# Kernel tuning notes

Hardware: AMD Instinct MI355X
Metric: run time of the kernel (lower is better)

Reference implementation:

```python
import jax, jax.numpy as jnp
import numpy as np

N, P = 65536, 1024

def setup_inputs() -> dict:
    key = jax.random.key(0)
    k1, k2, k3, k4 = jax.random.split(key, 4)
    X = jax.random.normal(k1, (N, P), dtype=jnp.float32)
    beta0 = jax.random.normal(k2, (1,), dtype=jnp.float32)
    beta = jax.random.normal(k3, (P,), dtype=jnp.float32)
    Theta = jax.random.normal(k4, (P, P), dtype=jnp.float32)
    return {"X": X, "beta0": beta0, "beta": beta, "Theta": Theta}

def reference(X, beta0, beta, Theta):
    # y_hat = beta0 + X @ beta + sum_{j<k} Theta[j,k] * X[:,j] * X[:,k]
    # The double loop uses only the strictly upper-triangular part of Theta.
    p = Theta.shape[0]
    theta_upper = jnp.triu(Theta, k=1)                     # [p, p]
    linear = beta0 + X @ beta                              # [n]
    interaction = jnp.sum((X @ theta_upper) * X, axis=1)   # [n], quadratic form
    return linear + interaction
```

## Files before the change

kernel.cpp:

```cpp
#include <hip/hip_runtime.h>


typedef __bf16 bf16_t;
typedef bf16_t bf16x8 __attribute__((ext_vector_type(8)));
typedef float f32x4 __attribute__((ext_vector_type(4)));
typedef unsigned short u16;
typedef u16 u16x4 __attribute__((ext_vector_type(4)));
typedef u16 u16x8 __attribute__((ext_vector_type(8)));

#define N_ROWS 65536
#define P_DIM  1024
#define BM 128
#define BN 128
#define BK 32

static __device__ __forceinline__ u16 f2bf(float f) {
  unsigned u = __builtin_bit_cast(unsigned, f);
  u += 0x7FFFu + ((u >> 16) & 1u);
  return (u16)(u >> 16);
}

static __device__ __forceinline__ void gload16(const void* g, void* lds_base) {
  __builtin_amdgcn_global_load_lds(
      (const __attribute__((address_space(1))) unsigned char*)g,
      (__attribute__((address_space(3))) unsigned char*)lds_base, 16, 0, 0);
}

__global__ void __launch_bounds__(256)
init_y(float* __restrict__ y, const float* __restrict__ beta0) {
  int i = blockIdx.x * blockDim.x + threadIdx.x;
  if (i < N_ROWS) y[i] = beta0[0];
}

__global__ void __launch_bounds__(128)
conv_theta(const float* __restrict__ Theta, u16* __restrict__ Tt,
           float* __restrict__ y, const float* __restrict__ beta0) {
  __shared__ float tile[32][33];
  const int tid = threadIdx.x;
  const int tg  = (blockIdx.y * gridDim.x + blockIdx.x) * 128 + tid;
  if (tg < N_ROWS) y[tg] = beta0[0];

  const int k0  = blockIdx.x * 32;
  const int c0  = blockIdx.y * 32;
  {
    const int tx = tid & 31;
    const int rb = tid >> 5;
    #pragma unroll
    for (int i = 0; i < 8; ++i) {
      int kl = rb * 8 + i;
      tile[kl][tx] = Theta[(size_t)(k0 + kl) * P_DIM + c0 + tx];
    }
  }
  __syncthreads();
  {
    const int cl = tid >> 2;
    const int qt = tid & 3;
    const int c  = c0 + cl;
    const int Q  = blockIdx.x * 4 + qt;
    u16x8 w;
    #pragma unroll
    for (int e = 0; e < 8; ++e) {
      int k = Q * 8 + e;
      float v = tile[qt * 8 + e][cl];
      w[e] = (k < c) ? f2bf(v) : (u16)0;
    }
    const int qs = (qt ^ ((c >> 1) & 3));
    *(u16x8*)(Tt + (size_t)c * P_DIM + (size_t)(blockIdx.x * 32 + qs * 8)) = w;
  }
}

__global__ void __launch_bounds__(512)
gemm_r18(const float* __restrict__ X, const u16* __restrict__ Tt,
         const float* __restrict__ beta, float* __restrict__ y)
{
  __shared__ __align__(16) u16 L[20480];

  const int nwg = (N_ROWS / BM) * (P_DIM / BN);
  const int swz = (blockIdx.x & 7) * (nwg / 8) + (blockIdx.x >> 3);
  const int bn  = 7 - (swz & 7);
  const int bm  = swz >> 3;
  const int c0  = bn * BN;
  const int m0  = bm * BM;
  const int nkt = (bn + 1) * 4;

  const int tid  = threadIdx.x;
  const int lane = tid & 63;
  const int wid  = tid >> 6;
  const int wm   = wid >> 1;
  const int wn   = wid & 1;
  const int l15  = lane & 15;
  const int lg   = lane >> 4;

  const int ar = tid >> 2;
  const int ap = tid & 3;
  const int aq = (ap ^ ((ar >> 1) & 3)) * 8;

  const int brow = wid * 16 + (lane >> 2);
  const int bq   = (lane & 3) * 8;

  f32x4 acc[2][4];
  #pragma unroll
  for (int i = 0; i < 2; ++i)
    #pragma unroll
    for (int j = 0; j < 4; ++j)
      acc[i][j] = (f32x4)0.0f;

  f32x4 av0, av1;

  #define STAGE_A_LOAD(t_)                                                      \
    {                                                                           \
      const float* s_ = X + (size_t)(m0 + ar) * P_DIM + (t_) * BK + ap * 8;     \
      av0 = ((const f32x4*)s_)[0];                                              \
      av1 = ((const f32x4*)s_)[1];                                              \
    }
  #define STAGE_A_WRITE(ab_)                                                    \
    {                                                                           \
      u16x8 w_;                                                                 \
      _Pragma("unroll")                                                         \
      for (int j = 0; j < 4; ++j) { w_[j] = f2bf(av0[j]); w_[j + 4] = f2bf(av1[j]); } \
      *(u16x8*)&L[(ab_) * 4096 + ar * 32 + aq] = w_;                            \
    }
  #define STAGE_B(bb_, t_)                                                      \
    gload16(Tt + (size_t)(c0 + brow) * P_DIM + (t_) * BK + bq,                  \
            &L[8192 + (bb_) * 4096 + wid * 512]);

  STAGE_B(0, 0)
  STAGE_B(1, 1)
  STAGE_A_LOAD(0)
  asm volatile("s_waitcnt vmcnt(0)" ::: "memory");
  __builtin_amdgcn_sched_barrier(0);
  STAGE_A_WRITE(0)
  asm volatile("s_waitcnt lgkmcnt(0)" ::: "memory");
  __builtin_amdgcn_sched_barrier(0);
  __builtin_amdgcn_s_barrier();
  __builtin_amdgcn_sched_barrier(0);

  for (int t = 0; t < nkt; ++t) {
    const int acur = t & 1;
    const int bcur = t % 3;
    const bool pre1 = (t + 1 < nkt);
    const bool pre2 = (t + 2 < nkt);
    if (pre1) STAGE_A_LOAD(t + 1)
    if (pre2) STAGE_B((t + 2) % 3, t + 2)

    bf16x8 af[2], bfr[4];
    #pragma unroll
    for (int mi = 0; mi < 2; ++mi) {
      const int rw = wm * 32 + mi * 16 + l15;
      u16x8 v = *(const u16x8*)&L[acur * 4096 + rw * 32 + (lg ^ ((rw >> 1) & 3)) * 8];
      af[mi] = __builtin_bit_cast(bf16x8, v);
    }
    #pragma unroll
    for (int ni = 0; ni < 4; ++ni) {
      const int cl = wn * 64 + ni * 16 + l15;
      u16x8 v = *(const u16x8*)&L[8192 + bcur * 4096 + cl * 32 + (lg ^ ((cl >> 1) & 3)) * 8];
      bfr[ni] = __builtin_bit_cast(bf16x8, v);
    }

    __builtin_amdgcn_s_setprio(1);
    #pragma unroll
    for (int mi = 0; mi < 2; ++mi)
      #pragma unroll
      for (int ni = 0; ni < 4; ++ni)
        acc[mi][ni] = __builtin_amdgcn_mfma_f32_16x16x32_bf16(bfr[ni], af[mi], acc[mi][ni], 0, 0, 0);
    __builtin_amdgcn_s_setprio(0);

    if (pre2) {
      asm volatile("s_waitcnt vmcnt(2)" ::: "memory");
    } else {
      asm volatile("s_waitcnt vmcnt(0)" ::: "memory");
    }
    __builtin_amdgcn_sched_barrier(0);
    if (pre1) STAGE_A_WRITE((t + 1) & 1)
    asm volatile("s_waitcnt lgkmcnt(0)" ::: "memory");
    __builtin_amdgcn_sched_barrier(0);
    __builtin_amdgcn_s_barrier();
    __builtin_amdgcn_sched_barrier(0);
  }
  #undef STAGE_A_LOAD
  #undef STAGE_A_WRITE
  #undef STAGE_B

  float ysum[2];
  ysum[0] = 0.0f; ysum[1] = 0.0f;

  #pragma unroll
  for (int mi = 0; mi < 2; ++mi) {
    const int row = m0 + wm * 32 + mi * 16 + l15;
    const float* xr = X + (size_t)row * P_DIM;
    #pragma unroll
    for (int ni = 0; ni < 4; ++ni) {
      const int cb = c0 + wn * 64 + ni * 16 + lg * 4;
      f32x4 xw = *(const f32x4*)(xr + cb);
      f32x4 bv = *(const f32x4*)(beta + cb);
      #pragma unroll
      for (int r = 0; r < 4; ++r)
        ysum[mi] += (acc[mi][ni][r] + bv[r]) * xw[r];
    }
  }

  #pragma unroll
  for (int mi = 0; mi < 2; ++mi) {
    ysum[mi] += __shfl_xor(ysum[mi], 16);
    ysum[mi] += __shfl_xor(ysum[mi], 32);
  }
  if (lane < 16) {
    #pragma unroll
    for (int mi = 0; mi < 2; ++mi)
      atomicAdd(&y[m0 + wm * 32 + mi * 16 + l15], ysum[mi]);
  }
}

#define LDT 40
__global__ void __launch_bounds__(256)
fused_quad_fallback(const float* __restrict__ X, const float* __restrict__ beta,
                    const float* __restrict__ Theta, float* __restrict__ y)
{
  __shared__ __align__(16) u16 Alds[128 * LDT];
  __shared__ __align__(16) u16 Blds[128 * LDT];

  const int bid = blockIdx.x;
  const int bn  = bid & 7;
  const int bm  = bid >> 3;
  const int c0  = bn * 128;
  const int m0  = bm * 128;
  const int nkt = (bn + 1) * 4;

  const int tid  = threadIdx.x;
  const int lane = tid & 63;
  const int wid  = tid >> 6;
  const int wm   = wid >> 1;
  const int wn   = wid & 1;
  const int l15  = lane & 15;
  const int lg   = lane >> 4;

  f32x4 acc[4][4];
  #pragma unroll
  for (int i = 0; i < 4; ++i)
    #pragma unroll
    for (int j = 0; j < 4; ++j)
      acc[i][j] = (f32x4)0.0f;

  const int arow  = tid >> 1;
  const int ahalf = (tid & 1) * 16;
  const int kb4 = (tid >> 5) * 4;
  const int cb4 = (tid & 31) * 4;

  for (int kt = 0; kt < nkt; ++kt) {
    const int k0 = kt * 32;
    __syncthreads();
    {
      const f32x4* p = (const f32x4*)(X + (size_t)(m0 + arow) * P_DIM + k0 + ahalf);
      f32x4 v0 = p[0], v1 = p[1], v2 = p[2], v3 = p[3];
      u16x8 w0, w1;
      #pragma unroll
      for (int i = 0; i < 4; ++i) {
        w0[i] = f2bf(v0[i]); w0[i + 4] = f2bf(v1[i]);
        w1[i] = f2bf(v2[i]); w1[i + 4] = f2bf(v3[i]);
      }
      *(u16x8*)&Alds[arow * LDT + ahalf]     = w0;
      *(u16x8*)&Alds[arow * LDT + ahalf + 8] = w1;
    }
    {
      float e[4][4];
      #pragma unroll
      for (int i = 0; i < 4; ++i) {
        f32x4 r = *(const f32x4*)(Theta + (size_t)(k0 + kb4 + i) * P_DIM + c0 + cb4);
        #pragma unroll
        for (int j = 0; j < 4; ++j)
          e[i][j] = ((k0 + kb4 + i) < (c0 + cb4 + j)) ? r[j] : 0.0f;
      }
      #pragma unroll
      for (int j = 0; j < 4; ++j) {
        u16x4 wv;
        #pragma unroll
        for (int i = 0; i < 4; ++i) wv[i] = f2bf(e[i][j]);
        *(u16x4*)&Blds[(cb4 + j) * LDT + kb4] = wv;
      }
    }
    __syncthreads();

    bf16x8 af[4], bfr[4];
    #pragma unroll
    for (int mi = 0; mi < 4; ++mi) {
      u16x8 t = *(const u16x8*)&Alds[(wm * 64 + mi * 16 + l15) * LDT + lg * 8];
      af[mi] = __builtin_bit_cast(bf16x8, t);
    }
    #pragma unroll
    for (int ni = 0; ni < 4; ++ni) {
      u16x8 t = *(const u16x8*)&Blds[(wn * 64 + ni * 16 + l15) * LDT + lg * 8];
      bfr[ni] = __builtin_bit_cast(bf16x8, t);
    }
    #pragma unroll
    for (int mi = 0; mi < 4; ++mi)
      #pragma unroll
      for (int ni = 0; ni < 4; ++ni)
        acc[mi][ni] = __builtin_amdgcn_mfma_f32_16x16x32_bf16(af[mi], bfr[ni], acc[mi][ni], 0, 0, 0);
  }

  float ysum[4][4];
  #pragma unroll
  for (int mi = 0; mi < 4; ++mi)
    #pragma unroll
    for (int r = 0; r < 4; ++r)
      ysum[mi][r] = 0.0f;

  #pragma unroll
  for (int ni = 0; ni < 4; ++ni) {
    const int col = c0 + wn * 64 + ni * 16 + l15;
    const float bta = beta[col];
    #pragma unroll
    for (int mi = 0; mi < 4; ++mi) {
      const int rowb = m0 + wm * 64 + mi * 16 + lg * 4;
      #pragma unroll
      for (int r = 0; r < 4; ++r) {
        float xv = X[(size_t)(rowb + r) * P_DIM + col];
        ysum[mi][r] += (acc[mi][ni][r] + bta) * xv;
      }
    }
  }

  #pragma unroll
  for (int m = 1; m < 16; m <<= 1)
    #pragma unroll
    for (int mi = 0; mi < 4; ++mi)
      #pragma unroll
      for (int r = 0; r < 4; ++r)
        ysum[mi][r] += __shfl_xor(ysum[mi][r], m);

  if (l15 == 0) {
    #pragma unroll
    for (int mi = 0; mi < 4; ++mi)
      #pragma unroll
      for (int r = 0; r < 4; ++r)
        atomicAdd(&y[m0 + wm * 64 + mi * 16 + lg * 4 + r], ysum[mi][r]);
  }
}

extern "C" void kernel_launch(void* const* d_in, const int* in_sizes, int n_in,
                              void* d_out, int out_size, void* d_ws, size_t ws_size,
                              hipStream_t stream) {
  const float* X     = (const float*)d_in[0];
  const float* beta0 = (const float*)d_in[1];
  const float* beta  = (const float*)d_in[2];
  const float* Theta = (const float*)d_in[3];
  float* y = (float*)d_out;

  const size_t need = (size_t)P_DIM * P_DIM * 2;
  if (ws_size >= need) {
    u16* Tt = (u16*)d_ws;
    conv_theta<<<dim3(32, 32), 128, 0, stream>>>(Theta, Tt, y, beta0);
    gemm_r18<<<(N_ROWS / BM) * (P_DIM / BN), 512, 0, stream>>>(X, Tt, beta, y);
  } else {
    init_y<<<N_ROWS / 256, 256, 0, stream>>>(y, beta0);
    fused_quad_fallback<<<(N_ROWS / 128) * (P_DIM / 128), 256, 0, stream>>>(X, beta, Theta, y);
  }
}
```

Before: 163.5 us.

## Load X fragments directly into registers, dropping LDS staging of A

The A operand (rows of X) is now read by each wave straight from global memory into MFMA fragment registers and converted to bf16 in registers, instead of being staged through shared memory. This removes the LDS write, the lgkm wait and half the LDS allocation, which could allow higher occupancy. In exchange, waves sharing the same rows both fetch them, doubling X reads from cache, and each lane reads a strided row segment. The global-memory wait count is adjusted to match the new number of outstanding loads.

```diff
diff --git a/kernel.cpp b/kernel.cpp
--- a/kernel.cpp
+++ b/kernel.cpp
@@ -70,10 +70,10 @@
 }
 
 __global__ void __launch_bounds__(512)
-gemm_r18(const float* __restrict__ X, const u16* __restrict__ Tt,
+gemm_r20(const float* __restrict__ X, const u16* __restrict__ Tt,
          const float* __restrict__ beta, float* __restrict__ y)
 {
-  __shared__ __align__(16) u16 L[20480];
+  __shared__ __align__(16) u16 L[3 * 4096];
 
   const int nwg = (N_ROWS / BM) * (P_DIM / BN);
   const int swz = (blockIdx.x & 7) * (nwg / 8) + (blockIdx.x >> 3);
@@ -91,9 +91,8 @@
   const int l15  = lane & 15;
   const int lg   = lane >> 4;
 
-  const int ar = tid >> 2;
-  const int ap = tid & 3;
-  const int aq = (ap ^ ((ar >> 1) & 3)) * 8;
+  const float* xr0 = X + (size_t)(m0 + wm * 32 + l15) * P_DIM + lg * 8;
+  const float* xr1 = xr0 + 16 * P_DIM;
 
   const int brow = wid * 16 + (lane >> 2);
   const int bq   = (lane & 3) * 8;
@@ -105,55 +104,54 @@
     for (int j = 0; j < 4; ++j)
       acc[i][j] = (f32x4)0.0f;
 
-  f32x4 av0, av1;
-
-  #define STAGE_A_LOAD(t_)                                                      \
+  f32x4 av0, av1, av2, av3;
+
+  #define LOAD_A(t_)                                                            \
     {                                                                           \
-      const float* s_ = X + (size_t)(m0 + ar) * P_DIM + (t_) * BK + ap * 8;     \
-      av0 = ((const f32x4*)s_)[0];                                              \
-      av1 = ((const f32x4*)s_)[1];                                              \
-    }
-  #define STAGE_A_WRITE(ab_)                                                    \
-    {                                                                           \
-      u16x8 w_;                                                                 \
-      _Pragma("unroll")                                                         \
-      for (int j = 0; j < 4; ++j) { w_[j] = f2bf(av0[j]); w_[j + 4] = f2bf(av1[j]); } \
-      *(u16x8*)&L[(ab_) * 4096 + ar * 32 + aq] = w_;                            \
+      const float* p0_ = xr0 + (t_) * BK;                                       \
+      const float* p1_ = xr1 + (t_) * BK;                                       \
+      av0 = ((const f32x4*)p0_)[0];                                             \
+      av1 = ((const f32x4*)p0_)[1];                                             \
+      av2 = ((const f32x4*)p1_)[0];                                             \
+      av3 = ((const f32x4*)p1_)[1];                                             \
     }
   #define STAGE_B(bb_, t_)                                                      \
     gload16(Tt + (size_t)(c0 + brow) * P_DIM + (t_) * BK + bq,                  \
-            &L[8192 + (bb_) * 4096 + wid * 512]);
+            &L[(bb_) * 4096 + wid * 512]);
 
   STAGE_B(0, 0)
   STAGE_B(1, 1)
-  STAGE_A_LOAD(0)
+  LOAD_A(0)
   asm volatile("s_waitcnt vmcnt(0)" ::: "memory");
-  __builtin_amdgcn_sched_barrier(0);
-  STAGE_A_WRITE(0)
-  asm volatile("s_waitcnt lgkmcnt(0)" ::: "memory");
   __builtin_amdgcn_sched_barrier(0);
   __builtin_amdgcn_s_barrier();
   __builtin_amdgcn_sched_barrier(0);
 
   for (int t = 0; t < nkt; ++t) {
-    const int acur = t & 1;
     const int bcur = t % 3;
     const bool pre1 = (t + 1 < nkt);
     const bool pre2 = (t + 2 < nkt);
-    if (pre1) STAGE_A_LOAD(t + 1)
+
+    bf16x8 af[2];
+    {
+      u16x8 w0, w1;
+      #pragma unroll
+      for (int j = 0; j < 4; ++j) {
+        w0[j] = f2bf(av0[j]); w0[j + 4] = f2bf(av1[j]);
+        w1[j] = f2bf(av2[j]); w1[j + 4] = f2bf(av3[j]);
+      }
+      af[0] = __builtin_bit_cast(bf16x8, w0);
+      af[1] = __builtin_bit_cast(bf16x8, w1);
+    }
+
+    if (pre1) LOAD_A(t + 1)
     if (pre2) STAGE_B((t + 2) % 3, t + 2)
 
-    bf16x8 af[2], bfr[4];
-    #pragma unroll
-    for (int mi = 0; mi < 2; ++mi) {
-      const int rw = wm * 32 + mi * 16 + l15;
-      u16x8 v = *(const u16x8*)&L[acur * 4096 + rw * 32 + (lg ^ ((rw >> 1) & 3)) * 8];
-      af[mi] = __builtin_bit_cast(bf16x8, v);
-    }
+    bf16x8 bfr[4];
     #pragma unroll
     for (int ni = 0; ni < 4; ++ni) {
       const int cl = wn * 64 + ni * 16 + l15;
-      u16x8 v = *(const u16x8*)&L[8192 + bcur * 4096 + cl * 32 + (lg ^ ((cl >> 1) & 3)) * 8];
+      u16x8 v = *(const u16x8*)&L[bcur * 4096 + cl * 32 + (lg ^ ((cl >> 1) & 3)) * 8];
       bfr[ni] = __builtin_bit_cast(bf16x8, v);
     }
 
@@ -166,19 +164,15 @@
     __builtin_amdgcn_s_setprio(0);
 
     if (pre2) {
-      asm volatile("s_waitcnt vmcnt(2)" ::: "memory");
+      asm volatile("s_waitcnt vmcnt(1)" ::: "memory");
     } else {
       asm volatile("s_waitcnt vmcnt(0)" ::: "memory");
     }
-    __builtin_amdgcn_sched_barrier(0);
-    if (pre1) STAGE_A_WRITE((t + 1) & 1)
-    asm volatile("s_waitcnt lgkmcnt(0)" ::: "memory");
     __builtin_amdgcn_sched_barrier(0);
     __builtin_amdgcn_s_barrier();
     __builtin_amdgcn_sched_barrier(0);
   }
-  #undef STAGE_A_LOAD
-  #undef STAGE_A_WRITE
+  #undef LOAD_A
   #undef STAGE_B
 
   float ysum[2];
@@ -350,7 +344,7 @@
   if (ws_size >= need) {
     u16* Tt = (u16*)d_ws;
     conv_theta<<<dim3(32, 32), 128, 0, stream>>>(Theta, Tt, y, beta0);
-    gemm_r18<<<(N_ROWS / BM) * (P_DIM / BN), 512, 0, stream>>>(X, Tt, beta, y);
+    gemm_r20<<<(N_ROWS / BM) * (P_DIM / BN), 512, 0, stream>>>(X, Tt, beta, y);
   } else {
     init_y<<<N_ROWS / 256, 256, 0, stream>>>(y, beta0);
     fused_quad_fallback<<<(N_ROWS / 128) * (P_DIM / 128), 256, 0, stream>>>(X, beta, Theta, y);
```

New measurement: 433.4 us. 165% more time.
